# Performance work log

Hardware: AMD Instinct MI355X
Metric: run time of the kernel (lower is better)

## Reference

```python
import jax, jax.numpy as jnp
import numpy as np

EPS = 1e-08
SIGMA = 0.1
B = 1.0


def setup_inputs() -> dict:
    key = jax.random.key(0)
    k1, k2 = jax.random.split(key)
    N, C, H, W = 4, 256, 64, 64
    featureT = jax.random.normal(k1, (N, C, H, W), dtype=jnp.float32)
    featureI = jax.random.normal(k2, (N, C, H, W), dtype=jnp.float32)
    return {"featureT": featureT, "featureI": featureI}


def reference(featureT, featureI):
    N, C, H, W = featureT.shape
    # center both by target mean over (batch, spatial)
    meanT = featureT.mean(axis=(0, 2, 3), keepdims=True)
    fI = featureI - meanT
    fT = featureT - meanT
    # channel-wise L2 normalize
    fI = fI / (jnp.linalg.norm(fI, axis=1, keepdims=True) + EPS)
    fT = fT / (jnp.linalg.norm(fT, axis=1, keepdims=True) + EPS)
    # 1x1-patch conv2d == contraction over channels: sim[n, p, h, w]
    # where p indexes the flattened H*W spatial positions of the target.
    fT_flat = fT.reshape(N, C, H * W)  # [N, C, P]
    sim = jnp.einsum('nchw,ncp->nphw', fI, fT_flat)  # [N, P, H, W]
    raw_dist = (1.0 - sim) / 2.0
    # relative distances: divide by min over patch axis
    div = jnp.min(raw_dist, axis=1, keepdims=True)
    relative_dist = raw_dist / (div + EPS)
    # contextual similarity: exp-weight + sum-normalize over patch axis
    Wt = jnp.exp((B - relative_dist) / (SIGMA + EPS))
    W_sum = Wt.sum(axis=1, keepdims=True)
    CX = Wt / (W_sum + EPS)
    # max over spatial dims of featureI, mean over patches, -log, mean over batch
    CX = CX.max(axis=(2, 3))           # [N, P]
    CX = CX.mean(axis=1)               # [N]
    CX_loss = -jnp.log(CX + EPS)
    return jnp.mean(CX_loss)
```

## Files before the change

kernel.cpp:

```cpp
#include <hip/hip_runtime.h>
#include <cmath>


#define NB 4
#define CC 256
#define HW 4096
#define NQ0 8

static constexpr float kEPS = 1e-8f;
static constexpr float kSIG = 0.1f + 1e-8f;

typedef __attribute__((ext_vector_type(8)))  short short8;
typedef __attribute__((ext_vector_type(16))) float f32x16;

enum {
  OFF_MEAN = 0,
  OFF_CMAX = 256,
  OFF_WSUM = OFF_CMAX + NQ0*NB*HW,
  OFF_MAXV = OFF_WSUM + NQ0*NB*HW,
  OFF_GT   = OFF_MAXV + NB*HW,
  OFF_GI   = OFF_GT + NB*HW*CC/2,
  WS_FLOATS_FULL = OFF_GI + NB*HW*CC/2
};

static constexpr unsigned kEncNegInf = 0x007fffffu;

__device__ __forceinline__ unsigned enc_f32(float f) {
  const unsigned u = __float_as_uint(f);
  return (u & 0x80000000u) ? ~u : (u | 0x80000000u);
}
__device__ __forceinline__ float dec_f32(unsigned e) {
  const unsigned u = (e & 0x80000000u) ? (e & 0x7fffffffu) : ~e;
  return __uint_as_float(u);
}

__device__ __forceinline__ ushort cvt_bf16(float x) {
  unsigned u = __float_as_uint(x);
  unsigned r = (u + 0x7fffu + ((u >> 16) & 1u)) >> 16;
  return (ushort)r;
}

__device__ __forceinline__ void glds16(const ushort* g, ushort* l) {
  __builtin_amdgcn_global_load_lds(
      (const __attribute__((address_space(1))) unsigned*)g,
      (__attribute__((address_space(3))) unsigned*)l, 16, 0, 0);
}
__device__ __forceinline__ void s_bar()  { asm volatile("s_barrier" ::: "memory"); }
__device__ __forceinline__ void w_vm4()  { asm volatile("s_waitcnt vmcnt(4)" ::: "memory"); }
__device__ __forceinline__ void w_vm0()  { asm volatile("s_waitcnt vmcnt(0)" ::: "memory"); }
__device__ __forceinline__ void w_lgkm() { asm volatile("s_waitcnt lgkmcnt(0)" ::: "memory"); }

__device__ __forceinline__ float blockSum256(float v) {
  __shared__ float sh[4];
  const int lane = threadIdx.x & 63, wv = threadIdx.x >> 6;
  #pragma unroll
  for (int o = 32; o > 0; o >>= 1) v += __shfl_down(v, o, 64);
  __syncthreads();
  if (lane == 0) sh[wv] = v;
  __syncthreads();
  return sh[0] + sh[1] + sh[2] + sh[3];
}

__global__ __launch_bounds__(256) void k_mean9(const float* __restrict__ fT,
                                               float* __restrict__ ws) {
  const int c = blockIdx.x, t = threadIdx.x;
  float s = 0.f;
  for (int n = 0; n < NB; ++n) {
    const float* p = fT + (size_t)(n*CC + c)*HW;
    #pragma unroll
    for (int k = 0; k < 16; ++k) s += p[k*256 + t];
  }
  const float tot = blockSum256(s);
  if (t == 0) ws[OFF_MEAN + c] = tot * (1.0f/16384.0f);
}

__global__ __launch_bounds__(256) void k_prep9(const float* __restrict__ fT,
                                               const float* __restrict__ fI,
                                               float* __restrict__ ws) {
  __shared__ float stage[32][257];
  __shared__ float prt[8][32];
  __shared__ float sinv[32];
  const int t = threadIdx.x, l = t & 63;
  const int obid = blockIdx.x;
  int bid = obid;
  const int tensor = (bid >= 512); bid &= 511;
  const int n   = bid >> 7;
  const int r32 = bid & 127;
  const int p0  = r32 * 32;

  if (obid < 64)
    ((unsigned*)(ws + OFF_MAXV))[obid*256 + t] = kEncNegInf;

  const float* __restrict__ src = tensor ? fI : fT;
  ushort* __restrict__ dst = (ushort*)(ws + (tensor ? OFF_GI : OFF_GT));
  const float* __restrict__ mean = ws + OFF_MEAN;

  const int pl = t & 31, cg = t >> 5;
  float acc = 0.f;
  #pragma unroll
  for (int i = 0; i < 32; ++i) {
    const int c = cg*32 + i;
    const float v = src[((size_t)(n*CC + c))*HW + p0 + pl] - mean[c];
    stage[pl][c] = v;
    acc += v*v;
  }
  prt[cg][pl] = acc;
  __syncthreads();
  if (t < 32) {
    float s = 0.f;
    #pragma unroll
    for (int g = 0; g < 8; ++g) s += prt[g][t];
    sinv[t] = 1.0f/(sqrtf(s) + kEPS);
  }
  __syncthreads();

  const int w = t >> 6, lhi = l >> 5, m = l & 31;
  const float iv = sinv[m];
  #pragma unroll
  for (int i = 0; i < 4; ++i) {
    const int kc = w*4 + i;
    const int cb = kc*16 + lhi*8;
    short8 o;
    #pragma unroll
    for (int j = 0; j < 8; ++j)
      ((ushort*)&o)[j] = cvt_bf16(stage[m][cb + j] * iv);
    *(short8*)(dst + (((size_t)(n*128 + r32)*16 + kc) << 9) + l*8) = o;
  }
}


__global__ __launch_bounds__(256, 2) void k_gA(
    const ushort* __restrict__ gA, const ushort* __restrict__ gB,
    float* __restrict__ ws)
{
  __shared__ ushort Ab[2][8192];
  __shared__ float red2[256];

  const int t = threadIdx.x;
  const int w = t >> 6, l = t & 63;
  const int ln31 = l & 31;

  const int L = blockIdx.x;
  const int xcd = L & 7, g = L >> 3;
  const int nh = xcd*4 + (g & 3);
  const int cs = g >> 2;
  const int n = nh >> 3, h = nh & 7;
  const int col0 = cs * 256;

  const ushort* __restrict__ gAn = gA + ((size_t)(n*128 + h*16) << 13);

  #pragma unroll
  for (int i = 0; i < 4; ++i)
    glds16(gAn + (size_t)(i*256 + t)*8, &Ab[0][(i*256 + t)*8]);
  #pragma unroll
  for (int i = 0; i < 4; ++i)
    glds16(gAn + 8192 + (size_t)(i*256 + t)*8, &Ab[1][(i*256 + t)*8]);

  short8 breg0[16], breg1[16];
  {
    const int RB0 = cs*8 + w, RB1 = cs*8 + 4 + w;
    #pragma unroll
    for (int kc = 0; kc < 16; ++kc) {
      breg0[kc] = *(const short8*)(gB + (((size_t)(n*128 + RB0)*16 + kc) << 9) + l*8);
      breg1[kc] = *(const short8*)(gB + (((size_t)(n*128 + RB1)*16 + kc) << 9) + l*8);
    }
  }

  float run0 = -3.0e38f, run1 = -3.0e38f;

  for (int iter = 0; iter < 16; ++iter) {
    if (iter < 15) w_vm4(); else w_vm0();
    s_bar();

    const ushort* __restrict__ Abuf = &Ab[iter & 1][0];
    f32x16 acc0, acc1;
    #pragma unroll
    for (int e = 0; e < 16; ++e) { acc0[e] = 0.f; acc1[e] = 0.f; }
    #pragma unroll
    for (int kc = 0; kc < 16; ++kc) {
      const short8 a0 = *(const short8*)&Abuf[kc*512 + l*8];
      acc0 = __builtin_amdgcn_mfma_f32_32x32x16_bf16(a0, breg0[kc], acc0, 0, 0, 0);
      acc1 = __builtin_amdgcn_mfma_f32_32x32x16_bf16(a0, breg1[kc], acc1, 0, 0, 0);
    }
    w_lgkm();
    s_bar();
    if (iter + 2 < 16) {
      const ushort* __restrict__ src = gAn + (size_t)(iter + 2)*8192;
      ushort* __restrict__ dstl = &Ab[iter & 1][0];
      #pragma unroll
      for (int i = 0; i < 4; ++i)
        glds16(src + (size_t)(i*256 + t)*8, dstl + (i*256 + t)*8);
    }

    #pragma unroll
    for (int r = 0; r < 16; ++r) {
      run0 = fmaxf(run0, acc0[r]);
      run1 = fmaxf(run1, acc1[r]);
    }
  }

  run0 = fmaxf(run0, __shfl_xor(run0, 32, 64));
  run1 = fmaxf(run1, __shfl_xor(run1, 32, 64));
  if (l < 32) {
    red2[w*32 + ln31]       = run0;
    red2[128 + w*32 + ln31] = run1;
  }
  __syncthreads();
  ws[OFF_CMAX + h*(NB*HW) + n*HW + col0 + t] = red2[t];
}

__global__ __launch_bounds__(256, 2) void k_gB(
    const ushort* __restrict__ gA, const ushort* __restrict__ gB,
    float* __restrict__ ws)
{
  __shared__ ushort Ab[2][8192];
  __shared__ float red2[256];

  const int t = threadIdx.x;
  const int w = t >> 6, l = t & 63;
  const int ln31 = l & 31;

  const int L = blockIdx.x;
  const int xcd = L & 7, g = L >> 3;
  const int nh = xcd*4 + (g & 3);
  const int cs = g >> 2;
  const int n = nh >> 3, h = nh & 7;
  const int col0 = cs * 256;

  const ushort* __restrict__ gAn = gA + ((size_t)(n*128 + h*16) << 13);

  #pragma unroll
  for (int i = 0; i < 4; ++i)
    glds16(gAn + (size_t)(i*256 + t)*8, &Ab[0][(i*256 + t)*8]);
  #pragma unroll
  for (int i = 0; i < 4; ++i)
    glds16(gAn + 8192 + (size_t)(i*256 + t)*8, &Ab[1][(i*256 + t)*8]);

  float aq0, bq0, aq1, bq1;
  {
    const int q0 = col0 + w*32 + ln31;
    const int q1 = q0 + 128;
    float cm0 = -3.0e38f, cm1 = -3.0e38f;
    #pragma unroll
    for (int hh = 0; hh < NQ0; ++hh) {
      cm0 = fmaxf(cm0, ws[OFF_CMAX + hh*(NB*HW) + n*HW + q0]);
      cm1 = fmaxf(cm1, ws[OFF_CMAX + hh*(NB*HW) + n*HW + q1]);
    }
    const float i0 = 1.0f/(2.0f*(0.5f*(1.0f - cm0) + kEPS));
    const float i1 = 1.0f/(2.0f*(0.5f*(1.0f - cm1) + kEPS));
    bq0 = i0 / kSIG; aq0 = (1.0f - i0) / kSIG;
    bq1 = i1 / kSIG; aq1 = (1.0f - i1) / kSIG;
  }

  short8 breg0[16], breg1[16];
  {
    const int RB0 = cs*8 + w, RB1 = cs*8 + 4 + w;
    #pragma unroll
    for (int kc = 0; kc < 16; ++kc) {
      breg0[kc] = *(const short8*)(gB + (((size_t)(n*128 + RB0)*16 + kc) << 9) + l*8);
      breg1[kc] = *(const short8*)(gB + (((size_t)(n*128 + RB1)*16 + kc) << 9) + l*8);
    }
  }

  float ws0 = 0.f, ws1 = 0.f;

  for (int iter = 0; iter < 16; ++iter) {
    if (iter < 15) w_vm4(); else w_vm0();
    s_bar();

    const ushort* __restrict__ Abuf = &Ab[iter & 1][0];
    f32x16 acc0, acc1;
    #pragma unroll
    for (int e = 0; e < 16; ++e) { acc0[e] = 0.f; acc1[e] = 0.f; }
    #pragma unroll
    for (int kc = 0; kc < 16; ++kc) {
      const short8 a0 = *(const short8*)&Abuf[kc*512 + l*8];
      acc0 = __builtin_amdgcn_mfma_f32_32x32x16_bf16(a0, breg0[kc], acc0, 0, 0, 0);
      acc1 = __builtin_amdgcn_mfma_f32_32x32x16_bf16(a0, breg1[kc], acc1, 0, 0, 0);
    }
    w_lgkm();
    s_bar();
    if (iter + 2 < 16) {
      const ushort* __restrict__ src = gAn + (size_t)(iter + 2)*8192;
      ushort* __restrict__ dstl = &Ab[iter & 1][0];
      #pragma unroll
      for (int i = 0; i < 4; ++i)
        glds16(src + (size_t)(i*256 + t)*8, dstl + (i*256 + t)*8);
    }

    #pragma unroll
    for (int r = 0; r < 16; ++r) {
      ws0 += __expf(fmaf(bq0, acc0[r], aq0));
      ws1 += __expf(fmaf(bq1, acc1[r], aq1));
    }
  }

  ws0 += __shfl_xor(ws0, 32, 64);
  ws1 += __shfl_xor(ws1, 32, 64);
  if (l < 32) {
    red2[w*32 + ln31]       = ws0;
    red2[128 + w*32 + ln31] = ws1;
  }
  __syncthreads();
  ws[OFF_WSUM + h*(NB*HW) + n*HW + col0 + t] = red2[t];
}

__global__ __launch_bounds__(256, 2) void k_gC(
    const ushort* __restrict__ gA, const ushort* __restrict__ gB,
    float* __restrict__ ws)
{
  __shared__ ushort Ab[2][8192];
  __shared__ float gam_s[256], bet_s[256];
  __shared__ float stash[4][512];

  const int t = threadIdx.x;
  const int w = t >> 6, l = t & 63;
  const int ln31 = l & 31, lhi = l >> 5;

  const int L = blockIdx.x;
  const int xcd = L & 7, g = L >> 3;
  const int nh = xcd*4 + (g & 3);
  const int cs = g >> 2;
  const int n = nh >> 3, h = nh & 7;
  const int col0 = cs * 256;

  const ushort* __restrict__ gAn = gA + ((size_t)(n*128 + h*16) << 13);

  #pragma unroll
  for (int i = 0; i < 4; ++i)
    glds16(gAn + (size_t)(i*256 + t)*8, &Ab[0][(i*256 + t)*8]);
  #pragma unroll
  for (int i = 0; i < 4; ++i)
    glds16(gAn + 8192 + (size_t)(i*256 + t)*8, &Ab[1][(i*256 + t)*8]);

  {
    const int idx = n*HW + col0 + t;
    float cm = -3.0e38f;
    #pragma unroll
    for (int hh = 0; hh < NQ0; ++hh)
      cm = fmaxf(cm, ws[OFF_CMAX + hh*(NB*HW) + idx]);
    float sw = 0.f;
    #pragma unroll
    for (int hh = 0; hh < NQ0; ++hh)
      sw += ws[OFF_WSUM + hh*(NB*HW) + idx];
    const float i0 = 1.0f/(2.0f*(0.5f*(1.0f - cm) + kEPS));
    bet_s[t] = i0 / kSIG;
    gam_s[t] = (1.0f - i0) / kSIG - logf(sw + kEPS);
  }

  short8 breg0[16], breg1[16];
  {
    const int RB0 = cs*8 + w, RB1 = cs*8 + 4 + w;
    #pragma unroll
    for (int kc = 0; kc < 16; ++kc) {
      breg0[kc] = *(const short8*)(gB + (((size_t)(n*128 + RB0)*16 + kc) << 9) + l*8);
      breg1[kc] = *(const short8*)(gB + (((size_t)(n*128 + RB1)*16 + kc) << 9) + l*8);
    }
  }
  __syncthreads();

  for (int iter = 0; iter < 16; ++iter) {
    if (iter < 15) w_vm4(); else w_vm0();
    s_bar();

    const ushort* __restrict__ Abuf = &Ab[iter & 1][0];
    f32x16 accq0, accq1;
    #pragma unroll
    for (int e = 0; e < 16; ++e) { accq0[e] = 0.f; accq1[e] = 0.f; }
    #pragma unroll
    for (int kc = 0; kc < 16; ++kc) {
      const short8 a0 = *(const short8*)&Abuf[kc*512 + l*8];
      accq0 = __builtin_amdgcn_mfma_f32_32x32x16_bf16(breg0[kc], a0, accq0, 0, 0, 0);
      accq1 = __builtin_amdgcn_mfma_f32_32x32x16_bf16(breg1[kc], a0, accq1, 0, 0, 0);
    }
    w_lgkm();
    s_bar();
    if (iter + 2 < 16) {
      const ushort* __restrict__ src = gAn + (size_t)(iter + 2)*8192;
      ushort* __restrict__ dstl = &Ab[iter & 1][0];
      #pragma unroll
      for (int i = 0; i < 4; ++i)
        glds16(src + (size_t)(i*256 + t)*8, dstl + (i*256 + t)*8);
    }

    float m = -3.0e38f;
    #pragma unroll
    for (int r = 0; r < 16; ++r) {
      const int row = (r & 3) + 8*(r >> 2) + 4*lhi;
      const float g0v = gam_s[w*32 + row],       b0v = bet_s[w*32 + row];
      const float g1v = gam_s[128 + w*32 + row], b1v = bet_s[128 + w*32 + row];
      m = fmaxf(m, fmaf(b0v, accq0[r], g0v));
      m = fmaxf(m, fmaf(b1v, accq1[r], g1v));
    }
    m = fmaxf(m, __shfl_xor(m, 32, 64));
    if (l < 32) stash[w][iter*32 + ln31] = m;
  }

  __syncthreads();
  unsigned* __restrict__ MV = (unsigned*)(ws + OFF_MAXV) + n*HW + h*512;
  #pragma unroll
  for (int p = t; p < 512; p += 256) {
    const float m = fmaxf(fmaxf(stash[0][p], stash[1][p]),
                          fmaxf(stash[2][p], stash[3][p]));
    atomicMax(&MV[p], enc_f32(m));
  }
}

__global__ __launch_bounds__(256) void k_final9(const float* __restrict__ ws,
                                                float* __restrict__ out) {
  const int t = threadIdx.x;
  const unsigned* __restrict__ MV = (const unsigned*)(ws + OFF_MAXV);
  float loss = 0.f;
  for (int n = 0; n < NB; ++n) {
    float s = 0.f;
    for (int k = 0; k < 16; ++k)
      s += __expf(dec_f32(MV[n*HW + k*256 + t]));
    const float tot = blockSum256(s);
    loss += -logf(tot*(1.0f/4096.0f) + kEPS);
  }
  if (t == 0) out[0] = loss*0.25f;
}

extern "C" void kernel_launch(void* const* d_in, const int* in_sizes, int n_in,
                              void* d_out, int out_size, void* d_ws, size_t ws_size,
                              hipStream_t stream) {
  const float* fT = (const float*)d_in[0];
  const float* fI = (const float*)d_in[1];
  float* out = (float*)d_out;
  float* ws  = (float*)d_ws;

  const size_t need_full = (size_t)WS_FLOATS_FULL * sizeof(float);
  if (ws_size < need_full) return;

  const ushort* GT = (const ushort*)(ws + OFF_GT);
  const ushort* GI = (const ushort*)(ws + OFF_GI);
  k_mean9 <<<256,  256, 0, stream>>>(fT, ws);
  k_prep9 <<<1024, 256, 0, stream>>>(fT, fI, ws);
  k_gA    <<<512,  256, 0, stream>>>(GT, GI, ws);
  k_gB    <<<512,  256, 0, stream>>>(GT, GI, ws);
  k_gC    <<<512,  256, 0, stream>>>(GT, GI, ws);
  k_final9<<<1,    256, 0, stream>>>(ws, out);
}
```

Measured before the change: 173.1 us.

## Fuse all stages into one cooperative persistent kernel with grid syncs

Replaces the six separate kernel launches (mean, prep, three GEMM passes, final reduction) with a single cooperative kernel of 512 blocks that separates the stages with grid-wide barriers. This removes per-launch overhead and the idle gaps between dependent kernels. The prep stage now runs two tiles per block instead of one block per tile. Grid syncs add their own cost, and the kernel needs all 512 blocks co-resident at 2 blocks per CU. If the cooperative launch fails, it falls back to the old multi-kernel path.

```diff
diff --git a/kernel.cpp b/kernel.cpp
--- a/kernel.cpp
+++ b/kernel.cpp
@@ -1,5 +1,8 @@
 #include <hip/hip_runtime.h>
+#include <hip/hip_cooperative_groups.h>
 #include <cmath>
+
+namespace cg = cooperative_groups;
 
 
 #define NB 4
@@ -60,6 +63,334 @@
   __syncthreads();
   return sh[0] + sh[1] + sh[2] + sh[3];
 }
+
+__global__ __launch_bounds__(256, 2) void k_all(
+    const float* __restrict__ fT, const float* __restrict__ fI,
+    float* __restrict__ ws, float* __restrict__ out)
+{
+  __shared__ __align__(16) char smem[43008];
+  cg::grid_group gg = cg::this_grid();
+
+  const int t = threadIdx.x, l = t & 63;
+  const int w = t >> 6, ln31 = l & 31, lhi = l >> 5;
+  const int L = blockIdx.x;
+
+  if (L < 256) {
+    const int c = L;
+    float s = 0.f;
+    for (int n = 0; n < NB; ++n) {
+      const float* p = fT + (size_t)(n*CC + c)*HW;
+      #pragma unroll
+      for (int k = 0; k < 16; ++k) s += p[k*256 + t];
+    }
+    const float tot = blockSum256(s);
+    if (t == 0) ws[OFF_MEAN + c] = tot * (1.0f/16384.0f);
+  }
+  if (L < 64)
+    ((unsigned*)(ws + OFF_MAXV))[L*256 + t] = kEncNegInf;
+  gg.sync();
+
+  {
+    float* stage = (float*)smem;
+    float* prt   = (float*)(smem + 32896);
+    float* sinv  = (float*)(smem + 33920);
+    const float* __restrict__ mean = ws + OFF_MEAN;
+    for (int rep = 0; rep < 2; ++rep) {
+      __syncthreads();
+      int bid = L + rep*512;
+      const int tensor = (bid >= 512); bid &= 511;
+      const int n = bid >> 7, r32 = bid & 127, p0 = r32*32;
+      const float* __restrict__ src = tensor ? fI : fT;
+      ushort* __restrict__ dst = (ushort*)(ws + (tensor ? OFF_GI : OFF_GT));
+      const int pl = t & 31, cgp = t >> 5;
+      float acc = 0.f;
+      #pragma unroll
+      for (int i = 0; i < 32; ++i) {
+        const int c = cgp*32 + i;
+        const float v = src[((size_t)(n*CC + c))*HW + p0 + pl] - mean[c];
+        stage[pl*257 + c] = v;
+        acc += v*v;
+      }
+      prt[cgp*32 + pl] = acc;
+      __syncthreads();
+      if (t < 32) {
+        float s2 = 0.f;
+        #pragma unroll
+        for (int g2 = 0; g2 < 8; ++g2) s2 += prt[g2*32 + t];
+        sinv[t] = 1.0f/(sqrtf(s2) + kEPS);
+      }
+      __syncthreads();
+      const float iv = sinv[ln31];
+      #pragma unroll
+      for (int i = 0; i < 4; ++i) {
+        const int kc = w*4 + i;
+        const int cb = kc*16 + lhi*8;
+        short8 o;
+        #pragma unroll
+        for (int j = 0; j < 8; ++j)
+          ((ushort*)&o)[j] = cvt_bf16(stage[ln31*257 + cb + j] * iv);
+        *(short8*)(dst + (((size_t)(n*128 + r32)*16 + kc) << 9) + l*8) = o;
+      }
+    }
+  }
+  gg.sync();
+
+  const ushort* __restrict__ gA = (const ushort*)(ws + OFF_GT);
+  const ushort* __restrict__ gB = (const ushort*)(ws + OFF_GI);
+  const int xcd = L & 7, grp = L >> 3;
+  const int nh = xcd*4 + (grp & 3);
+  const int cs = grp >> 2;
+  const int n = nh >> 3, h = nh & 7;
+  const int col0 = cs * 256;
+  const ushort* __restrict__ gAn = gA + ((size_t)(n*128 + h*16) << 13);
+
+  {
+    ushort* Ab   = (ushort*)smem;
+    float*  red2 = (float*)(smem + 32768);
+
+    #pragma unroll
+    for (int i = 0; i < 4; ++i)
+      glds16(gAn + (size_t)(i*256 + t)*8, Ab + (i*256 + t)*8);
+    #pragma unroll
+    for (int i = 0; i < 4; ++i)
+      glds16(gAn + 8192 + (size_t)(i*256 + t)*8, Ab + 8192 + (i*256 + t)*8);
+
+    short8 breg0[16], breg1[16];
+    {
+      const int RB0 = cs*8 + w, RB1 = cs*8 + 4 + w;
+      #pragma unroll
+      for (int kc = 0; kc < 16; ++kc) {
+        breg0[kc] = *(const short8*)(gB + (((size_t)(n*128 + RB0)*16 + kc) << 9) + l*8);
+        breg1[kc] = *(const short8*)(gB + (((size_t)(n*128 + RB1)*16 + kc) << 9) + l*8);
+      }
+    }
+
+    float run0 = -3.0e38f, run1 = -3.0e38f;
+
+    for (int iter = 0; iter < 16; ++iter) {
+      if (iter < 15) w_vm4(); else w_vm0();
+      s_bar();
+
+      const ushort* __restrict__ Abuf = Ab + (iter & 1)*8192;
+      f32x16 acc0, acc1;
+      #pragma unroll
+      for (int e = 0; e < 16; ++e) { acc0[e] = 0.f; acc1[e] = 0.f; }
+      #pragma unroll
+      for (int kc = 0; kc < 16; ++kc) {
+        const short8 a0 = *(const short8*)&Abuf[kc*512 + l*8];
+        acc0 = __builtin_amdgcn_mfma_f32_32x32x16_bf16(a0, breg0[kc], acc0, 0, 0, 0);
+        acc1 = __builtin_amdgcn_mfma_f32_32x32x16_bf16(a0, breg1[kc], acc1, 0, 0, 0);
+      }
+      w_lgkm();
+      s_bar();
+      if (iter + 2 < 16) {
+        const ushort* __restrict__ src = gAn + (size_t)(iter + 2)*8192;
+        ushort* __restrict__ dstl = Ab + (iter & 1)*8192;
+        #pragma unroll
+        for (int i = 0; i < 4; ++i)
+          glds16(src + (size_t)(i*256 + t)*8, dstl + (i*256 + t)*8);
+      }
+
+      #pragma unroll
+      for (int r = 0; r < 16; ++r) {
+        run0 = fmaxf(run0, acc0[r]);
+        run1 = fmaxf(run1, acc1[r]);
+      }
+    }
+
+    run0 = fmaxf(run0, __shfl_xor(run0, 32, 64));
+    run1 = fmaxf(run1, __shfl_xor(run1, 32, 64));
+    if (l < 32) {
+      red2[w*32 + ln31]       = run0;
+      red2[128 + w*32 + ln31] = run1;
+    }
+    __syncthreads();
+    ws[OFF_CMAX + h*(NB*HW) + n*HW + col0 + t] = red2[t];
+  }
+  gg.sync();
+
+  {
+    ushort* Ab   = (ushort*)smem;
+    float*  red2 = (float*)(smem + 32768);
+
+    #pragma unroll
+    for (int i = 0; i < 4; ++i)
+      glds16(gAn + (size_t)(i*256 + t)*8, Ab + (i*256 + t)*8);
+    #pragma unroll
+    for (int i = 0; i < 4; ++i)
+      glds16(gAn + 8192 + (size_t)(i*256 + t)*8, Ab + 8192 + (i*256 + t)*8);
+
+    float aq0, bq0, aq1, bq1;
+    {
+      const int q0 = col0 + w*32 + ln31;
+      const int q1 = q0 + 128;
+      float cm0 = -3.0e38f, cm1 = -3.0e38f;
+      #pragma unroll
+      for (int hh = 0; hh < NQ0; ++hh) {
+        cm0 = fmaxf(cm0, ws[OFF_CMAX + hh*(NB*HW) + n*HW + q0]);
+        cm1 = fmaxf(cm1, ws[OFF_CMAX + hh*(NB*HW) + n*HW + q1]);
+      }
+      const float i0 = 1.0f/(2.0f*(0.5f*(1.0f - cm0) + kEPS));
+      const float i1 = 1.0f/(2.0f*(0.5f*(1.0f - cm1) + kEPS));
+      bq0 = i0 / kSIG; aq0 = (1.0f - i0) / kSIG;
+      bq1 = i1 / kSIG; aq1 = (1.0f - i1) / kSIG;
+    }
+
+    short8 breg0[16], breg1[16];
+    {
+      const int RB0 = cs*8 + w, RB1 = cs*8 + 4 + w;
+      #pragma unroll
+      for (int kc = 0; kc < 16; ++kc) {
+        breg0[kc] = *(const short8*)(gB + (((size_t)(n*128 + RB0)*16 + kc) << 9) + l*8);
+        breg1[kc] = *(const short8*)(gB + (((size_t)(n*128 + RB1)*16 + kc) << 9) + l*8);
+      }
+    }
+
+    float ws0 = 0.f, ws1 = 0.f;
+
+    for (int iter = 0; iter < 16; ++iter) {
+      if (iter < 15) w_vm4(); else w_vm0();
+      s_bar();
+
+      const ushort* __restrict__ Abuf = Ab + (iter & 1)*8192;
+      f32x16 acc0, acc1;
+      #pragma unroll
+      for (int e = 0; e < 16; ++e) { acc0[e] = 0.f; acc1[e] = 0.f; }
+      #pragma unroll
+      for (int kc = 0; kc < 16; ++kc) {
+        const short8 a0 = *(const short8*)&Abuf[kc*512 + l*8];
+        acc0 = __builtin_amdgcn_mfma_f32_32x32x16_bf16(a0, breg0[kc], acc0, 0, 0, 0);
+        acc1 = __builtin_amdgcn_mfma_f32_32x32x16_bf16(a0, breg1[kc], acc1, 0, 0, 0);
+      }
+      w_lgkm();
+      s_bar();
+      if (iter + 2 < 16) {
+        const ushort* __restrict__ src = gAn + (size_t)(iter + 2)*8192;
+        ushort* __restrict__ dstl = Ab + (iter & 1)*8192;
+        #pragma unroll
+        for (int i = 0; i < 4; ++i)
+          glds16(src + (size_t)(i*256 + t)*8, dstl + (i*256 + t)*8);
+      }
+
+      #pragma unroll
+      for (int r = 0; r < 16; ++r) {
+        ws0 += __expf(fmaf(bq0, acc0[r], aq0));
+        ws1 += __expf(fmaf(bq1, acc1[r], aq1));
+      }
+    }
+
+    ws0 += __shfl_xor(ws0, 32, 64);
+    ws1 += __shfl_xor(ws1, 32, 64);
+    if (l < 32) {
+      red2[w*32 + ln31]       = ws0;
+      red2[128 + w*32 + ln31] = ws1;
+    }
+    __syncthreads();
+    ws[OFF_WSUM + h*(NB*HW) + n*HW + col0 + t] = red2[t];
+  }
+  gg.sync();
+
+  {
+    ushort* Ab    = (ushort*)smem;
+    float*  gam_s = (float*)(smem + 32768);
+    float*  bet_s = (float*)(smem + 33792);
+    float*  stash = (float*)(smem + 34816);
+
+    #pragma unroll
+    for (int i = 0; i < 4; ++i)
+      glds16(gAn + (size_t)(i*256 + t)*8, Ab + (i*256 + t)*8);
+    #pragma unroll
+    for (int i = 0; i < 4; ++i)
+      glds16(gAn + 8192 + (size_t)(i*256 + t)*8, Ab + 8192 + (i*256 + t)*8);
+
+    {
+      const int idx = n*HW + col0 + t;
+      float cm = -3.0e38f;
+      #pragma unroll
+      for (int hh = 0; hh < NQ0; ++hh)
+        cm = fmaxf(cm, ws[OFF_CMAX + hh*(NB*HW) + idx]);
+      float sw = 0.f;
+      #pragma unroll
+      for (int hh = 0; hh < NQ0; ++hh)
+        sw += ws[OFF_WSUM + hh*(NB*HW) + idx];
+      const float i0 = 1.0f/(2.0f*(0.5f*(1.0f - cm) + kEPS));
+      bet_s[t] = i0 / kSIG;
+      gam_s[t] = (1.0f - i0) / kSIG - logf(sw + kEPS);
+    }
+
+    short8 breg0[16], breg1[16];
+    {
+      const int RB0 = cs*8 + w, RB1 = cs*8 + 4 + w;
+      #pragma unroll
+      for (int kc = 0; kc < 16; ++kc) {
+        breg0[kc] = *(const short8*)(gB + (((size_t)(n*128 + RB0)*16 + kc) << 9) + l*8);
+        breg1[kc] = *(const short8*)(gB + (((size_t)(n*128 + RB1)*16 + kc) << 9) + l*8);
+      }
+    }
+    __syncthreads();
+
+    for (int iter = 0; iter < 16; ++iter) {
+      if (iter < 15) w_vm4(); else w_vm0();
+      s_bar();
+
+      const ushort* __restrict__ Abuf = Ab + (iter & 1)*8192;
+      f32x16 accq0, accq1;
+      #pragma unroll
+      for (int e = 0; e < 16; ++e) { accq0[e] = 0.f; accq1[e] = 0.f; }
+      #pragma unroll
+      for (int kc = 0; kc < 16; ++kc) {
+        const short8 a0 = *(const short8*)&Abuf[kc*512 + l*8];
+        accq0 = __builtin_amdgcn_mfma_f32_32x32x16_bf16(breg0[kc], a0, accq0, 0, 0, 0);
+        accq1 = __builtin_amdgcn_mfma_f32_32x32x16_bf16(breg1[kc], a0, accq1, 0, 0, 0);
+      }
+      w_lgkm();
+      s_bar();
+      if (iter + 2 < 16) {
+        const ushort* __restrict__ src = gAn + (size_t)(iter + 2)*8192;
+        ushort* __restrict__ dstl = Ab + (iter & 1)*8192;
+        #pragma unroll
+        for (int i = 0; i < 4; ++i)
+          glds16(src + (size_t)(i*256 + t)*8, dstl + (i*256 + t)*8);
+      }
+
+      float m = -3.0e38f;
+      #pragma unroll
+      for (int r = 0; r < 16; ++r) {
+        const int row = (r & 3) + 8*(r >> 2) + 4*lhi;
+        const float g0v = gam_s[w*32 + row],       b0v = bet_s[w*32 + row];
+        const float g1v = gam_s[128 + w*32 + row], b1v = bet_s[128 + w*32 + row];
+        m = fmaxf(m, fmaf(b0v, accq0[r], g0v));
+        m = fmaxf(m, fmaf(b1v, accq1[r], g1v));
+      }
+      m = fmaxf(m, __shfl_xor(m, 32, 64));
+      if (l < 32) stash[w*512 + iter*32 + ln31] = m;
+    }
+
+    __syncthreads();
+    unsigned* __restrict__ MV = (unsigned*)(ws + OFF_MAXV) + n*HW + h*512;
+    #pragma unroll
+    for (int p = t; p < 512; p += 256) {
+      const float m = fmaxf(fmaxf(stash[0*512 + p], stash[1*512 + p]),
+                            fmaxf(stash[2*512 + p], stash[3*512 + p]));
+      atomicMax(&MV[p], enc_f32(m));
+    }
+  }
+  gg.sync();
+
+  if (L == 0) {
+    const unsigned* __restrict__ MV = (const unsigned*)(ws + OFF_MAXV);
+    float loss = 0.f;
+    for (int nn = 0; nn < NB; ++nn) {
+      float s = 0.f;
+      for (int k = 0; k < 16; ++k)
+        s += __expf(dec_f32(MV[nn*HW + k*256 + t]));
+      const float tot = blockSum256(s);
+      loss += -logf(tot*(1.0f/4096.0f) + kEPS);
+    }
+    if (t == 0) out[0] = loss*0.25f;
+  }
+}
+
 
 __global__ __launch_bounds__(256) void k_mean9(const float* __restrict__ fT,
                                                float* __restrict__ ws) {
@@ -128,7 +459,6 @@
   }
 }
 
-
 __global__ __launch_bounds__(256, 2) void k_gA(
     const ushort* __restrict__ gA, const ushort* __restrict__ gB,
     float* __restrict__ ws)
@@ -432,6 +762,13 @@
   const size_t need_full = (size_t)WS_FLOATS_FULL * sizeof(float);
   if (ws_size < need_full) return;
 
+  {
+    void* args[] = {(void*)&fT, (void*)&fI, (void*)&ws, (void*)&out};
+    if (hipLaunchCooperativeKernel((const void*)k_all, dim3(512), dim3(256),
+                                   args, 0, stream) == hipSuccess)
+      return;
+  }
+
   const ushort* GT = (const ushort*)(ws + OFF_GT);
   const ushort* GI = (const ushort*)(ws + OFF_GI);
   k_mean9 <<<256,  256, 0, stream>>>(fT, ws);
```

Measured after the change: 433.6 us. 2.51x slower.
